# Optimization experiments

Hardware: AMD Instinct MI355X
Metric: run time of the kernel (lower is better)

## Reference

```python
import jax, jax.numpy as jnp
import numpy as np

T, B, D, H = 1024, 8, 1024, 16
NH = D // H  # 64, per-head width (nhid)
W_SCALE = 0.02


def setup_inputs() -> dict:
    key = jax.random.key(0)
    ks = jax.random.split(key, 10)
    return {
        "input_tensor": jax.random.normal(ks[0], (T, B, D), jnp.float32),
        "keys_vector": jax.random.normal(ks[1], (T, B, D), jnp.float32),
        "values_vector": jax.random.normal(ks[2], (T, B, D), jnp.float32),
        # per-head projection weights: [H, D, NH]
        "Wq": jax.random.normal(ks[3], (H, D, NH), jnp.float32) * W_SCALE,
        "bq": jnp.zeros((H, NH), jnp.float32),
        "Wk": jax.random.normal(ks[4], (H, D, NH), jnp.float32) * W_SCALE,
        "bk": jnp.zeros((H, NH), jnp.float32),
        "Wv": jax.random.normal(ks[5], (H, D, NH), jnp.float32) * W_SCALE,
        "bv": jnp.zeros((H, NH), jnp.float32),
        # output projection after concatenating heads
        "Wo": jax.random.normal(ks[6], (D, D), jnp.float32) * W_SCALE,
        "bo": jnp.zeros((D,), jnp.float32),
        "mask": 1,  # True: causal (growing key slice per timestep)
    }


def reference(input_tensor, keys_vector, values_vector, Wq, bq, Wk, bk, Wv, bv, Wo, bo, mask):
    # Vectorized equivalent of the per-timestep loop: query at step t attends
    # to keys/values[:t+1] when mask is set, else to the full sequence.
    q = jnp.einsum('tbd,hdk->tbhk', input_tensor, Wq) + bq   # [T,B,H,NH]
    k = jnp.einsum('sbd,hdk->sbhk', keys_vector, Wk) + bk    # [T,B,H,NH]
    v = jnp.einsum('sbd,hdk->sbhk', values_vector, Wv) + bv  # [T,B,H,NH]

    scale = 1.0 / jnp.sqrt(jnp.float32(NH))
    scores = jnp.einsum('tbhk,sbhk->bhts', q, k) * scale     # [B,H,T,T]
    if mask:
        causal = jnp.tril(jnp.ones((T, T), dtype=bool))      # s <= t
        scores = jnp.where(causal[None, None], scores, jnp.float32(-1e9))
    attn = jax.nn.softmax(scores, axis=-1)                   # over key dim s

    out = jnp.einsum('bhts,sbhk->tbhk', attn, v)             # [T,B,H,NH]
    out = out.reshape(T, B, D)                               # concat heads
    return out @ Wo.T + bo                                   # [T,B,D]
```

## Files before the change

### kernel.cpp

```cpp
#include <hip/hip_runtime.h>

typedef short bf16x8 __attribute__((ext_vector_type(8)));
typedef float f32x4 __attribute__((ext_vector_type(4)));
typedef float f32x16 __attribute__((ext_vector_type(16)));

typedef const __attribute__((address_space(1))) void* gptr_t;
typedef __attribute__((address_space(3))) void* sptr_t;

#define Z16 {0.f,0.f,0.f,0.f,0.f,0.f,0.f,0.f,0.f,0.f,0.f,0.f,0.f,0.f,0.f,0.f}
#define VMCNT(n) asm volatile("s_waitcnt vmcnt(" #n ")" ::: "memory")
#define LGKM0 asm volatile("s_waitcnt lgkmcnt(0)" ::: "memory")
#define SCHEDB __builtin_amdgcn_sched_barrier(0)
#define SBAR __builtin_amdgcn_s_barrier()

__device__ __forceinline__ void glds16(const void* g, void* s) {
  __builtin_amdgcn_global_load_lds((gptr_t)g, (sptr_t)s, 16, 0, 0);
}

__device__ __forceinline__ unsigned short f2bf(float x) {
  unsigned u = __float_as_uint(x);
  u = u + 0x7fffu + ((u >> 16) & 1u);
  return (unsigned short)(u >> 16);
}

__device__ __forceinline__ unsigned packbf(float lo, float hi) {
  return (unsigned)f2bf(lo) | (((unsigned)f2bf(hi)) << 16);
}

__global__ __launch_bounds__(256) void prep(const float* __restrict__ X,
                                            const float* __restrict__ KY,
                                            const float* __restrict__ VY,
                                            const float* __restrict__ Wo,
                                            const float* __restrict__ Wq,
                                            const float* __restrict__ Wk,
                                            const float* __restrict__ Wv,
                                            unsigned short* __restrict__ XB,
                                            unsigned short* __restrict__ WOB,
                                            unsigned short* __restrict__ WT) {
  __shared__ float tile[64][65];
  if (blockIdx.x < 2048) {
    int stride = 2048 * 256;
    for (int i = blockIdx.x * 256 + threadIdx.x; i < 6553600; i += stride) {
      const float* in; unsigned short* out; int k;
      if (i < 2097152)      { in = X;  out = XB;            k = i; }
      else if (i < 4194304) { in = KY; out = XB + 8388608;  k = i - 2097152; }
      else if (i < 6291456) { in = VY; out = XB + 16777216; k = i - 4194304; }
      else                  { in = Wo; out = WOB;           k = i - 6291456; }
      float4 v = ((const float4*)in)[k];
      uint2 r;
      r.x = packbf(v.x, v.y);
      r.y = packbf(v.z, v.w);
      ((uint2*)out)[k] = r;
    }
    return;
  }
  int idx = blockIdx.x - 2048;
  int bx = idx & 15, by = idx >> 4;
  int m = by >> 4, h = by & 15, d0 = bx * 64;
  const float* src = (m == 0 ? Wq : (m == 1 ? Wk : Wv)) + (size_t)h * 65536;
  int c = (threadIdx.x & 15) * 4, r0 = threadIdx.x >> 4;
#pragma unroll
  for (int rr = 0; rr < 4; ++rr) {
    int dr = rr * 16 + r0;
    float4 v = *(const float4*)(src + (size_t)(d0 + dr) * 64 + c);
    tile[dr][c + 0] = v.x; tile[dr][c + 1] = v.y;
    tile[dr][c + 2] = v.z; tile[dr][c + 3] = v.w;
  }
  __syncthreads();
#pragma unroll
  for (int rr = 0; rr < 4; ++rr) {
    int kr = rr * 16 + r0;
    uint2 pk;
    pk.x = packbf(tile[c + 0][kr], tile[c + 1][kr]);
    pk.y = packbf(tile[c + 2][kr], tile[c + 3][kr]);
    *(uint2*)(WT + ((size_t)(m * 1024 + h * 64 + kr)) * 1024 + d0 + c) = pk;
  }
}

__global__ __launch_bounds__(256) void gemm_qkv(const unsigned short* __restrict__ Ab,
                                                const unsigned short* __restrict__ Bb,
                                                const float* __restrict__ bi0,
                                                const float* __restrict__ bi1,
                                                const float* __restrict__ bi2,
                                                unsigned short* __restrict__ outp) {
  const int K = 1024;
  int z = blockIdx.z;
  const unsigned short* A = Ab + (size_t)z * 8192 * 1024;
  const unsigned short* BT = Bb + (size_t)z * 1024 * 1024;
  const float* bias = z == 0 ? bi0 : (z == 1 ? bi1 : bi2);
  int lin = blockIdx.y * 64 + blockIdx.x;
  int mt = (lin & 7) * 8 + ((lin >> 3) & 7);
  int nt = lin >> 6;
  int m0 = mt * 128, n0 = nt * 128;
  __shared__ __align__(16) char lds[65536];
  int tid = threadIdx.x, w = tid >> 6, l = tid & 63, ml = l & 15, hi = l >> 4;
  int wr = (w >> 1) * 64, wc = (w & 1) * 64;
  int srow = l >> 3;
  int kphys = (l & 7) << 4;
  f32x4 acc[4][4] = {};
#pragma unroll
  for (int i = 0; i < 4; ++i) {
    int c = w * 4 + i;
    int row = c * 8 + srow;
    int klog = kphys ^ ((row & 7) << 4);
    glds16((const char*)(A + (size_t)(m0 + row) * K) + klog, lds + c * 1024);
    glds16((const char*)(BT + (size_t)(n0 + row) * K) + klog, lds + 16384 + c * 1024);
  }
  __syncthreads();
  int cur = 0;
  for (int kt16 = 0; kt16 < 16; ++kt16) {
    if (kt16 + 1 < 16) {
      char* nb = lds + (cur ^ 1) * 32768;
      int kt = (kt16 + 1) * 64;
#pragma unroll
      for (int i = 0; i < 4; ++i) {
        int c = w * 4 + i;
        int row = c * 8 + srow;
        int klog = kphys ^ ((row & 7) << 4);
        glds16((const char*)(A + (size_t)(m0 + row) * K + kt) + klog, nb + c * 1024);
        glds16((const char*)(BT + (size_t)(n0 + row) * K + kt) + klog, nb + 16384 + c * 1024);
      }
    }
    char* As = lds + cur * 32768;
    char* Bs = As + 16384;
#pragma unroll
    for (int ks = 0; ks < 2; ++ks) {
      bf16x8 af[4], bfr[4];
#pragma unroll
      for (int mi = 0; mi < 4; ++mi) {
        int row = wr + mi * 16 + ml;
        af[mi] = *(const bf16x8*)(As + row * 128 + ((ks * 64 + (hi << 4)) ^ ((row & 7) << 4)));
      }
#pragma unroll
      for (int ni = 0; ni < 4; ++ni) {
        int row = wc + ni * 16 + ml;
        bfr[ni] = *(const bf16x8*)(Bs + row * 128 + ((ks * 64 + (hi << 4)) ^ ((row & 7) << 4)));
      }
      __builtin_amdgcn_s_setprio(1);
#pragma unroll
      for (int mi = 0; mi < 4; ++mi)
#pragma unroll
        for (int ni = 0; ni < 4; ++ni)
          acc[mi][ni] = __builtin_amdgcn_mfma_f32_16x16x32_bf16(af[mi], bfr[ni], acc[mi][ni], 0, 0, 0);
      __builtin_amdgcn_s_setprio(0);
    }
    __syncthreads();
    cur ^= 1;
  }
#pragma unroll
  for (int mi = 0; mi < 4; ++mi) {
#pragma unroll
    for (int ni = 0; ni < 4; ++ni) {
      int col = wc + ni * 16 + ml;
      float bv = bias[n0 + col];
#pragma unroll
      for (int r = 0; r < 4; ++r) {
        int row = wr + mi * 16 + (hi << 2) + r;
        float v = acc[mi][ni][r] + bv;
        float pv = __shfl_xor(v, 1);
        unsigned pk = (ml & 1) ? packbf(pv, v) : packbf(v, pv);
        *(unsigned*)(lds + row * 256 + (((col * 2) & ~3) ^ ((row & 7) << 4))) = pk;
      }
    }
  }
  __syncthreads();
  unsigned short* ob = outp + (size_t)z * 8388608;
  if (z != 2) {
    int rr = tid >> 1, hh = tid & 1;
    int t = (m0 + rr) >> 3, b = (m0 + rr) & 7;
    int hg = (n0 >> 6) + hh;
    unsigned short* dst = ob + (size_t)(b * 16 + hg) * 65536 + (size_t)t * 64;
#pragma unroll
    for (int j = 0; j < 8; ++j) {
      uint4 d = *(uint4*)(lds + rr * 256 + ((hh * 128 + j * 16) ^ ((rr & 7) << 4)));
      *(uint4*)(dst + j * 8) = d;
    }
  } else {
    int t0 = m0 >> 3;
#pragma unroll
    for (int q = 0; q < 4; ++q) {
      int run = q * 256 + tid;
      int k = run & 63;
      int bh2 = run >> 6;
      int b = bh2 >> 1, hh = bh2 & 1;
      int colb = (hh * 64 + k) * 2;
      union { unsigned short u[16]; uint4 v[2]; } tmp;
#pragma unroll
      for (int tp = 0; tp < 16; ++tp) {
        int rowt = tp * 8 + b;
        tmp.u[tp] = *(unsigned short*)(lds + rowt * 256 + (colb ^ ((b & 7) << 4)));
      }
      int hg = (n0 >> 6) + hh;
      unsigned short* dst = ob + (size_t)(b * 16 + hg) * 65536 + (size_t)k * 1024 + t0;
      *(uint4*)dst = tmp.v[0];
      *(uint4*)(dst + 8) = tmp.v[1];
    }
  }
}

__global__ __launch_bounds__(256) void gemm_out(const unsigned short* __restrict__ A,
                                                const unsigned short* __restrict__ BT,
                                                const float* __restrict__ bias,
                                                float* __restrict__ outp) {
  const int K = 1024;
  int lin = blockIdx.y * 64 + blockIdx.x;
  int mt = (lin & 7) * 8 + ((lin >> 3) & 7);
  int nt = lin >> 6;
  int m0 = mt * 128, n0 = nt * 128;
  __shared__ __align__(16) char lds[65536];
  int tid = threadIdx.x, w = tid >> 6, l = tid & 63, ml = l & 15, hi = l >> 4;
  int wr = (w >> 1) * 64, wc = (w & 1) * 64;
  int srow = l >> 3;
  int kphys = (l & 7) << 4;
  f32x4 acc[4][4] = {};
#pragma unroll
  for (int i = 0; i < 4; ++i) {
    int c = w * 4 + i;
    int row = c * 8 + srow;
    int klog = kphys ^ ((row & 7) << 4);
    glds16((const char*)(A + (size_t)(m0 + row) * K) + klog, lds + c * 1024);
    glds16((const char*)(BT + (size_t)(n0 + row) * K) + klog, lds + 16384 + c * 1024);
  }
  __syncthreads();
  int cur = 0;
  for (int kt16 = 0; kt16 < 16; ++kt16) {
    if (kt16 + 1 < 16) {
      char* nb = lds + (cur ^ 1) * 32768;
      int kt = (kt16 + 1) * 64;
#pragma unroll
      for (int i = 0; i < 4; ++i) {
        int c = w * 4 + i;
        int row = c * 8 + srow;
        int klog = kphys ^ ((row & 7) << 4);
        glds16((const char*)(A + (size_t)(m0 + row) * K + kt) + klog, nb + c * 1024);
        glds16((const char*)(BT + (size_t)(n0 + row) * K + kt) + klog, nb + 16384 + c * 1024);
      }
    }
    char* As = lds + cur * 32768;
    char* Bs = As + 16384;
#pragma unroll
    for (int ks = 0; ks < 2; ++ks) {
      bf16x8 af[4], bfr[4];
#pragma unroll
      for (int mi = 0; mi < 4; ++mi) {
        int row = wr + mi * 16 + ml;
        af[mi] = *(const bf16x8*)(As + row * 128 + ((ks * 64 + (hi << 4)) ^ ((row & 7) << 4)));
      }
#pragma unroll
      for (int ni = 0; ni < 4; ++ni) {
        int row = wc + ni * 16 + ml;
        bfr[ni] = *(const bf16x8*)(Bs + row * 128 + ((ks * 64 + (hi << 4)) ^ ((row & 7) << 4)));
      }
      __builtin_amdgcn_s_setprio(1);
#pragma unroll
      for (int mi = 0; mi < 4; ++mi)
#pragma unroll
        for (int ni = 0; ni < 4; ++ni)
          acc[mi][ni] = __builtin_amdgcn_mfma_f32_16x16x32_bf16(af[mi], bfr[ni], acc[mi][ni], 0, 0, 0);
      __builtin_amdgcn_s_setprio(0);
    }
    __syncthreads();
    cur ^= 1;
  }
#pragma unroll
  for (int mi = 0; mi < 4; ++mi) {
#pragma unroll
    for (int ni = 0; ni < 4; ++ni) {
      int col = n0 + wc + ni * 16 + ml;
      float bv = bias[col];
#pragma unroll
      for (int r = 0; r < 4; ++r) {
        int row = m0 + wr + mi * 16 + (hi << 2) + r;
        outp[(size_t)row * 1024 + col] = acc[mi][ni][r] + bv;
      }
    }
  }
}

__global__ __launch_bounds__(128, 2) void attn_k(const unsigned short* __restrict__ Qp,
                                                 const unsigned short* __restrict__ Kp,
                                                 const unsigned short* __restrict__ VTp,
                                                 unsigned short* __restrict__ Op,
                                                 const int* __restrict__ maskp) {
  int lin = blockIdx.x;
  int xcd = lin & 7, idx = lin >> 3;
  int bh = xcd + 8 * (idx & 15);
  int s = 15 - (idx >> 4);
  const size_t base = (size_t)bh * 65536;
  int tid = threadIdx.x, w = tid >> 6, l = tid & 63;
  int ml5 = l & 31, hi1 = l >> 5;
  int tw0 = s * 64 + w * 32;
  int t_glob = tw0 + ml5;
  __shared__ __align__(16) char lds[32768];
  int msk = *maskp;
  const float CE = 0.18033688011112042f;
  bf16x8 bq[4];
#pragma unroll
  for (int kd = 0; kd < 4; ++kd)
    bq[kd] = *(const bf16x8*)(Qp + base + (size_t)t_glob * 64 + kd * 16 + hi1 * 8);
  f32x16 o0 = Z16, o1 = Z16;
  float m_run = -3e38f, l_run = 0.f;
  int lim = msk ? s : 15;
  int srow = l >> 3, kphys = (l & 7) << 4;
  int klog = kphys ^ (srow << 4);
  int swz = (ml5 & 7) << 4;
  if (w == 0) {
#pragma unroll
    for (int i = 0; i < 8; ++i) {
      int row = i * 8 + srow;
      glds16((const char*)(Kp + base + (size_t)row * 64) + klog, lds + i * 1024);
    }
  } else {
#pragma unroll
    for (int i = 0; i < 8; ++i) {
      int row = i * 8 + srow;
      glds16((const char*)(VTp + base + (size_t)row * 1024) + klog, lds + 8192 + i * 1024);
    }
  }
  int cur = 0;
  for (int st = 0; st <= lim; ++st) {
    if (st < lim) {
      char* nb = lds + (cur ^ 1) * 16384;
      if (w == 0) {
#pragma unroll
        for (int i = 0; i < 8; ++i) {
          int row = i * 8 + srow;
          glds16((const char*)(Kp + base + (size_t)((st + 1) * 64 + row) * 64) + klog, nb + i * 1024);
        }
      } else {
#pragma unroll
        for (int i = 0; i < 8; ++i) {
          int row = i * 8 + srow;
          glds16((const char*)(VTp + base + (size_t)row * 1024 + (st + 1) * 64) + klog, nb + 8192 + i * 1024);
        }
      }
      VMCNT(8);
    } else {
      VMCNT(0);
    }
    SCHEDB; SBAR; SCHEDB;
    char* Ks = lds + cur * 16384;
    char* Vs = Ks + 8192;
    f32x16 s0 = Z16, s1 = Z16;
    __builtin_amdgcn_s_setprio(1);
#pragma unroll
    for (int kd = 0; kd < 4; ++kd) {
      int koff = kd * 32 + hi1 * 16;
      bf16x8 a0 = *(const bf16x8*)(Ks + ml5 * 128 + (koff ^ swz));
      bf16x8 a1 = *(const bf16x8*)(Ks + (32 + ml5) * 128 + (koff ^ swz));
      s0 = __builtin_amdgcn_mfma_f32_32x32x16_bf16(a0, bq[kd], s0, 0, 0, 0);
      s1 = __builtin_amdgcn_mfma_f32_32x32x16_bf16(a1, bq[kd], s1, 0, 0, 0);
    }
    __builtin_amdgcn_s_setprio(0);
    if (msk && st == s) {
#pragma unroll
      for (int r = 0; r < 16; ++r) {
        int sl = st * 64 + (r & 3) + 8 * (r >> 2) + 4 * hi1;
        if (sl > t_glob) s0[r] = -1e30f;
        if (sl + 32 > t_glob) s1[r] = -1e30f;
      }
    }
    float t8[8];
#pragma unroll
    for (int r = 0; r < 8; ++r)
      t8[r] = fmaxf(fmaxf(s0[r], s0[r + 8]), fmaxf(s1[r], s1[r + 8]));
    float tm = fmaxf(fmaxf(fmaxf(t8[0], t8[1]), fmaxf(t8[2], t8[3])),
                     fmaxf(fmaxf(t8[4], t8[5]), fmaxf(t8[6], t8[7])));
    tm = fmaxf(tm, __shfl_xor(tm, 32));
    if (!__all(tm <= m_run + 8.0f)) {
      float m_new = fmaxf(m_run, tm);
      float sc2 = exp2f((m_run - m_new) * CE);
      l_run *= sc2;
#pragma unroll
      for (int r = 0; r < 16; ++r) { o0[r] *= sc2; o1[r] *= sc2; }
      m_run = m_new;
    }
    float mC = m_run * CE;
#pragma unroll
    for (int r = 0; r < 16; ++r) {
      s0[r] = exp2f(fmaf(s0[r], CE, -mC));
      s1[r] = exp2f(fmaf(s1[r], CE, -mC));
    }
    float a8[8];
#pragma unroll
    for (int r = 0; r < 8; ++r)
      a8[r] = (s0[r] + s0[r + 8]) + (s1[r] + s1[r + 8]);
    float ps = ((a8[0] + a8[1]) + (a8[2] + a8[3])) + ((a8[4] + a8[5]) + (a8[6] + a8[7]));
    ps += __shfl_xor(ps, 32);
    l_run += ps;
    unsigned cc0[4][2], cc1[4][2];
#pragma unroll
    for (int q = 0; q < 4; ++q) {
      cc0[q][0] = packbf(s0[4 * q + 0], s0[4 * q + 1]);
      cc0[q][1] = packbf(s0[4 * q + 2], s0[4 * q + 3]);
      cc1[q][0] = packbf(s1[4 * q + 0], s1[4 * q + 1]);
      cc1[q][1] = packbf(s1[4 * q + 2], s1[4 * q + 3]);
    }
#define CCa(a, p) ((a) < 4 ? cc0[(a) & 3][p] : cc1[(a) & 3][p])
    union U4 { unsigned u[4]; bf16x8 v; };
    bf16x8 pb[4];
#pragma unroll
    for (int kb = 0; kb < 4; ++kb) {
      U4 t;
#pragma unroll
      for (int p = 0; p < 2; ++p) {
        unsigned x = CCa(2 * kb, p), y = CCa(2 * kb + 1, p);
        unsigned v = hi1 ? x : y;
        unsigned wv = hi1 ? y : x;
        unsigned vs = __shfl_xor(v, 32);
        t.u[p]     = hi1 ? vs : wv;
        t.u[2 + p] = hi1 ? wv : vs;
      }
      pb[kb] = t.v;
    }
#undef CCa
    __builtin_amdgcn_s_setprio(1);
#pragma unroll
    for (int kb = 0; kb < 4; ++kb) {
      int koff = kb * 32 + hi1 * 16;
      bf16x8 v0 = *(const bf16x8*)(Vs + ml5 * 128 + (koff ^ swz));
      bf16x8 v1 = *(const bf16x8*)(Vs + (32 + ml5) * 128 + (koff ^ swz));
      o0 = __builtin_amdgcn_mfma_f32_32x32x16_bf16(v0, pb[kb], o0, 0, 0, 0);
      o1 = __builtin_amdgcn_mfma_f32_32x32x16_bf16(v1, pb[kb], o1, 0, 0, 0);
    }
    __builtin_amdgcn_s_setprio(0);
    SCHEDB; LGKM0; SBAR;
    cur ^= 1;
  }
  float rl = 1.0f / l_run;
  int b = bh >> 4, h = bh & 15;
  unsigned short* orow = Op + (size_t)(t_glob * 8 + b) * 1024 + h * 64;
#pragma unroll
  for (int q2 = 0; q2 < 4; ++q2) {
    uint2 pk0, pk1;
    pk0.x = packbf(o0[4 * q2 + 0] * rl, o0[4 * q2 + 1] * rl);
    pk0.y = packbf(o0[4 * q2 + 2] * rl, o0[4 * q2 + 3] * rl);
    *(uint2*)(orow + 4 * hi1 + 8 * q2) = pk0;
    pk1.x = packbf(o1[4 * q2 + 0] * rl, o1[4 * q2 + 1] * rl);
    pk1.y = packbf(o1[4 * q2 + 2] * rl, o1[4 * q2 + 3] * rl);
    *(uint2*)(orow + 32 + 4 * hi1 + 8 * q2) = pk1;
  }
}

extern "C" void kernel_launch(void* const* d_in, const int* in_sizes, int n_in,
                              void* d_out, int out_size, void* d_ws, size_t ws_size,
                              hipStream_t stream) {
  const float* X  = (const float*)d_in[0];
  const float* KY = (const float*)d_in[1];
  const float* VY = (const float*)d_in[2];
  const float* Wq = (const float*)d_in[3];
  const float* bq = (const float*)d_in[4];
  const float* Wk = (const float*)d_in[5];
  const float* bk = (const float*)d_in[6];
  const float* Wv = (const float*)d_in[7];
  const float* bv = (const float*)d_in[8];
  const float* Wo = (const float*)d_in[9];
  const float* bo = (const float*)d_in[10];
  const int* mask = (const int*)d_in[11];
  char* ws = (char*)d_ws;
  unsigned short* XB  = (unsigned short*)(ws);
  unsigned short* WT  = (unsigned short*)(ws + 48ll * 1024 * 1024);
  unsigned short* WOB = (unsigned short*)(ws + 54ll * 1024 * 1024);
  unsigned short* QP  = (unsigned short*)(ws + 56ll * 1024 * 1024);
  unsigned short* OP  = (unsigned short*)(ws + 104ll * 1024 * 1024);

  prep<<<2816, 256, 0, stream>>>(X, KY, VY, Wo, Wq, Wk, Wv, XB, WOB, WT);
  gemm_qkv<<<dim3(64, 8, 3), 256, 0, stream>>>(XB, WT, bq, bk, bv, QP);
  attn_k<<<2048, 128, 0, stream>>>(QP, QP + 8388608, QP + 16777216, OP, mask);
  gemm_out<<<dim3(64, 8, 1), 256, 0, stream>>>(OP, WOB, bo, (float*)d_out);
}
```

Baseline: 185.5 us.

## Rewrite QKV GEMM as 256x256 tile, 8-wave, half-tile staged pipeline

Replaces the 128x128, 4-wave, double-buffered QKV projection GEMM with a 256x256 tile using 8 waves and 128 KB of dynamic LDS. Loads are split into half-tile stages that are interleaved with four MFMA quadrants, using explicit vmcnt and lgkmcnt waits and barriers so global-to-LDS prefetch overlaps compute. Larger tiles raise data reuse per LDS byte. The cost is only 384 blocks, lower occupancy and more barriers per K step. The epilogue is rescaled to the wider tile.

```diff
diff --git a/kernel.cpp b/kernel.cpp
--- a/kernel.cpp
+++ b/kernel.cpp
@@ -77,123 +77,164 @@
   }
 }
 
-__global__ __launch_bounds__(256) void gemm_qkv(const unsigned short* __restrict__ Ab,
-                                                const unsigned short* __restrict__ Bb,
-                                                const float* __restrict__ bi0,
-                                                const float* __restrict__ bi1,
-                                                const float* __restrict__ bi2,
-                                                unsigned short* __restrict__ outp) {
+__global__ __launch_bounds__(512, 2) void gemm_qkv8(const unsigned short* __restrict__ Ab,
+                                                    const unsigned short* __restrict__ Bb,
+                                                    const float* __restrict__ bi0,
+                                                    const float* __restrict__ bi1,
+                                                    const float* __restrict__ bi2,
+                                                    unsigned short* __restrict__ outp) {
+  extern __shared__ __align__(16) char lds[];
   const int K = 1024;
   int z = blockIdx.z;
   const unsigned short* A = Ab + (size_t)z * 8192 * 1024;
   const unsigned short* BT = Bb + (size_t)z * 1024 * 1024;
   const float* bias = z == 0 ? bi0 : (z == 1 ? bi1 : bi2);
-  int lin = blockIdx.y * 64 + blockIdx.x;
-  int mt = (lin & 7) * 8 + ((lin >> 3) & 7);
-  int nt = lin >> 6;
-  int m0 = mt * 128, n0 = nt * 128;
-  __shared__ __align__(16) char lds[65536];
-  int tid = threadIdx.x, w = tid >> 6, l = tid & 63, ml = l & 15, hi = l >> 4;
-  int wr = (w >> 1) * 64, wc = (w & 1) * 64;
+  int m0 = blockIdx.x * 256, n0 = blockIdx.y * 256;
+  int tid = threadIdx.x, wid = tid >> 6, l = tid & 63, ml = l & 15, hi = l >> 4;
+  int wr = (wid >> 2) * 128, wc = (wid & 3) * 64;
   int srow = l >> 3;
-  int kphys = (l & 7) << 4;
-  f32x4 acc[4][4] = {};
-#pragma unroll
-  for (int i = 0; i < 4; ++i) {
-    int c = w * 4 + i;
-    int row = c * 8 + srow;
-    int klog = kphys ^ ((row & 7) << 4);
-    glds16((const char*)(A + (size_t)(m0 + row) * K) + klog, lds + c * 1024);
-    glds16((const char*)(BT + (size_t)(n0 + row) * K) + klog, lds + 16384 + c * 1024);
+  int ksw = ((l & 7) << 4) ^ (srow << 4);
+  f32x4 acc[8][4] = {};
+  auto STG = [&](int mat, int h, int T, int d) {
+    const unsigned short* src = mat ? BT : A;
+    int rc0 = mat ? n0 : m0;
+    char* dst = lds + d * 65536 + mat * 32768 + h * 16384;
+#pragma unroll
+    for (int i = 0; i < 2; ++i) {
+      int c = wid * 2 + i;
+      int row = h * 128 + c * 8 + srow;
+      glds16((const char*)(src + (size_t)(rc0 + row) * K + T * 64) + ksw, dst + c * 1024);
+    }
+  };
+  auto RDA = [&](bf16x8 (&af)[4][2], int mg, int d) {
+    char* As = lds + d * 65536;
+#pragma unroll
+    for (int mf = 0; mf < 4; ++mf)
+#pragma unroll
+      for (int ks = 0; ks < 2; ++ks) {
+        int row = wr + mg * 64 + mf * 16 + ml;
+        af[mf][ks] = *(const bf16x8*)(As + row * 128 + ((ks * 64 + (hi << 4)) ^ ((row & 7) << 4)));
+      }
+  };
+  auto RDB = [&](bf16x8 (&bf)[2][2], int ng, int d) {
+    char* Bs = lds + d * 65536 + 32768;
+#pragma unroll
+    for (int nf = 0; nf < 2; ++nf)
+#pragma unroll
+      for (int ks = 0; ks < 2; ++ks) {
+        int row = wc + ng * 32 + nf * 16 + ml;
+        bf[nf][ks] = *(const bf16x8*)(Bs + row * 128 + ((ks * 64 + (hi << 4)) ^ ((row & 7) << 4)));
+      }
+  };
+  auto MM = [&](bf16x8 (&af)[4][2], bf16x8 (&bf)[2][2], int mg, int ng) {
+    __builtin_amdgcn_s_setprio(1);
+#pragma unroll
+    for (int ks = 0; ks < 2; ++ks)
+#pragma unroll
+      for (int mf = 0; mf < 4; ++mf)
+#pragma unroll
+        for (int nf = 0; nf < 2; ++nf)
+          acc[mg * 4 + mf][ng * 2 + nf] = __builtin_amdgcn_mfma_f32_16x16x32_bf16(
+              af[mf][ks], bf[nf][ks], acc[mg * 4 + mf][ng * 2 + nf], 0, 0, 0);
+    __builtin_amdgcn_s_setprio(0);
+  };
+  STG(0, 0, 0, 0); STG(0, 1, 0, 0); STG(1, 0, 0, 0); STG(1, 1, 0, 0);
+  STG(1, 0, 1, 1); STG(1, 1, 1, 1);
+  VMCNT(4); SCHEDB; SBAR;
+  for (int j = 0; j < 8; ++j) {
+    int b = 2 * j + 1, T2 = 2 * j + 2, T3 = 2 * j + 3;
+    bool s2 = T2 < 16, s3 = T3 < 16;
+    bf16x8 a03[4][2], a47[4][2], b01[2][2], b23[2][2];
+    RDA(a03, 0, 0); RDB(b01, 0, 0);
+    STG(0, 0, b, 1);
+    SCHEDB; SBAR; LGKM0; SCHEDB;
+    MM(a03, b01, 0, 0);
+    SCHEDB; SBAR;
+    RDB(b23, 1, 0);
+    STG(0, 1, b, 1);
+    SCHEDB; SBAR; LGKM0; SCHEDB;
+    MM(a03, b23, 0, 1);
+    SCHEDB; SBAR;
+    RDA(a47, 1, 0);
+    if (s2) STG(1, 0, T2, 0);
+    SCHEDB; SBAR; LGKM0; SCHEDB;
+    MM(a47, b23, 1, 1);
+    SCHEDB; SBAR;
+    if (s2) STG(1, 1, T2, 0);
+    SCHEDB; SBAR; LGKM0; SCHEDB;
+    MM(a47, b01, 1, 0);
+    if (j < 7) { VMCNT(4); } else { VMCNT(0); }
+    SCHEDB; SBAR;
+    RDA(a03, 0, 1); RDB(b01, 0, 1);
+    if (s2) STG(0, 0, T2, 0);
+    SCHEDB; SBAR; LGKM0; SCHEDB;
+    MM(a03, b01, 0, 0);
+    SCHEDB; SBAR;
+    RDB(b23, 1, 1);
+    if (s2) STG(0, 1, T2, 0);
+    SCHEDB; SBAR; LGKM0; SCHEDB;
+    MM(a03, b23, 0, 1);
+    SCHEDB; SBAR;
+    RDA(a47, 1, 1);
+    if (s3) STG(1, 0, T3, 1);
+    SCHEDB; SBAR; LGKM0; SCHEDB;
+    MM(a47, b23, 1, 1);
+    SCHEDB; SBAR;
+    if (s3) STG(1, 1, T3, 1);
+    SCHEDB; SBAR; LGKM0; SCHEDB;
+    MM(a47, b01, 1, 0);
+    if (j < 7) { VMCNT(4); } else { VMCNT(0); }
+    SCHEDB; SBAR;
   }
   __syncthreads();
-  int cur = 0;
-  for (int kt16 = 0; kt16 < 16; ++kt16) {
-    if (kt16 + 1 < 16) {
-      char* nb = lds + (cur ^ 1) * 32768;
-      int kt = (kt16 + 1) * 64;
-#pragma unroll
-      for (int i = 0; i < 4; ++i) {
-        int c = w * 4 + i;
-        int row = c * 8 + srow;
-        int klog = kphys ^ ((row & 7) << 4);
-        glds16((const char*)(A + (size_t)(m0 + row) * K + kt) + klog, nb + c * 1024);
-        glds16((const char*)(BT + (size_t)(n0 + row) * K + kt) + klog, nb + 16384 + c * 1024);
-      }
-    }
-    char* As = lds + cur * 32768;
-    char* Bs = As + 16384;
-#pragma unroll
-    for (int ks = 0; ks < 2; ++ks) {
-      bf16x8 af[4], bfr[4];
-#pragma unroll
-      for (int mi = 0; mi < 4; ++mi) {
-        int row = wr + mi * 16 + ml;
-        af[mi] = *(const bf16x8*)(As + row * 128 + ((ks * 64 + (hi << 4)) ^ ((row & 7) << 4)));
-      }
-#pragma unroll
-      for (int ni = 0; ni < 4; ++ni) {
-        int row = wc + ni * 16 + ml;
-        bfr[ni] = *(const bf16x8*)(Bs + row * 128 + ((ks * 64 + (hi << 4)) ^ ((row & 7) << 4)));
-      }
-      __builtin_amdgcn_s_setprio(1);
-#pragma unroll
-      for (int mi = 0; mi < 4; ++mi)
-#pragma unroll
-        for (int ni = 0; ni < 4; ++ni)
-          acc[mi][ni] = __builtin_amdgcn_mfma_f32_16x16x32_bf16(af[mi], bfr[ni], acc[mi][ni], 0, 0, 0);
-      __builtin_amdgcn_s_setprio(0);
-    }
-    __syncthreads();
-    cur ^= 1;
-  }
-#pragma unroll
-  for (int mi = 0; mi < 4; ++mi) {
-#pragma unroll
-    for (int ni = 0; ni < 4; ++ni) {
-      int col = wc + ni * 16 + ml;
-      float bv = bias[n0 + col];
+#pragma unroll
+  for (int nf = 0; nf < 4; ++nf) {
+    int col = wc + nf * 16 + ml;
+    float bv = bias[n0 + col];
+#pragma unroll
+    for (int mf = 0; mf < 8; ++mf)
 #pragma unroll
       for (int r = 0; r < 4; ++r) {
-        int row = wr + mi * 16 + (hi << 2) + r;
-        float v = acc[mi][ni][r] + bv;
+        int row = wr + mf * 16 + (hi << 2) + r;
+        float v = acc[mf][nf][r] + bv;
         float pv = __shfl_xor(v, 1);
         unsigned pk = (ml & 1) ? packbf(pv, v) : packbf(v, pv);
-        *(unsigned*)(lds + row * 256 + (((col * 2) & ~3) ^ ((row & 7) << 4))) = pk;
-      }
-    }
+        *(unsigned*)(lds + row * 512 + (((col * 2) & ~3) ^ ((row & 7) << 4))) = pk;
+      }
   }
   __syncthreads();
   unsigned short* ob = outp + (size_t)z * 8388608;
   if (z != 2) {
-    int rr = tid >> 1, hh = tid & 1;
-    int t = (m0 + rr) >> 3, b = (m0 + rr) & 7;
-    int hg = (n0 >> 6) + hh;
-    unsigned short* dst = ob + (size_t)(b * 16 + hg) * 65536 + (size_t)t * 64;
-#pragma unroll
-    for (int j = 0; j < 8; ++j) {
-      uint4 d = *(uint4*)(lds + rr * 256 + ((hh * 128 + j * 16) ^ ((rr & 7) << 4)));
-      *(uint4*)(dst + j * 8) = d;
+#pragma unroll
+    for (int q = 0; q < 2; ++q) {
+      int id = q * 512 + tid;
+      int rr = id >> 2, hh = id & 3;
+      int t = (m0 + rr) >> 3, b2 = (m0 + rr) & 7;
+      int h = (n0 >> 6) + hh;
+      unsigned short* dst = ob + (size_t)(b2 * 16 + h) * 65536 + (size_t)t * 64;
+#pragma unroll
+      for (int jj = 0; jj < 8; ++jj) {
+        uint4 d = *(uint4*)(lds + rr * 512 + ((hh * 128 + jj * 16) ^ ((rr & 7) << 4)));
+        *(uint4*)(dst + jj * 8) = d;
+      }
     }
   } else {
     int t0 = m0 >> 3;
 #pragma unroll
     for (int q = 0; q < 4; ++q) {
-      int run = q * 256 + tid;
-      int k = run & 63;
-      int bh2 = run >> 6;
-      int b = bh2 >> 1, hh = bh2 & 1;
+      int id = q * 512 + tid;
+      int k = id & 63;
+      int bh2 = id >> 6;
+      int b2 = bh2 >> 2, hh = bh2 & 3;
       int colb = (hh * 64 + k) * 2;
-      union { unsigned short u[16]; uint4 v[2]; } tmp;
-#pragma unroll
-      for (int tp = 0; tp < 16; ++tp) {
-        int rowt = tp * 8 + b;
-        tmp.u[tp] = *(unsigned short*)(lds + rowt * 256 + (colb ^ ((b & 7) << 4)));
-      }
-      int hg = (n0 >> 6) + hh;
-      unsigned short* dst = ob + (size_t)(b * 16 + hg) * 65536 + (size_t)k * 1024 + t0;
-      *(uint4*)dst = tmp.v[0];
-      *(uint4*)(dst + 8) = tmp.v[1];
+      union { unsigned short u[32]; uint4 v[4]; } tmp;
+#pragma unroll
+      for (int tp = 0; tp < 32; ++tp)
+        tmp.u[tp] = *(unsigned short*)(lds + (tp * 8 + b2) * 512 + (colb ^ (b2 << 4)));
+      int h = (n0 >> 6) + hh;
+      unsigned short* dst = ob + (size_t)(b2 * 16 + h) * 65536 + (size_t)k * 1024 + t0;
+#pragma unroll
+      for (int jj = 0; jj < 4; ++jj) *(uint4*)(dst + jj * 8) = tmp.v[jj];
     }
   }
 }
@@ -465,7 +506,7 @@
   unsigned short* OP  = (unsigned short*)(ws + 104ll * 1024 * 1024);
 
   prep<<<2816, 256, 0, stream>>>(X, KY, VY, Wo, Wq, Wk, Wv, XB, WOB, WT);
-  gemm_qkv<<<dim3(64, 8, 3), 256, 0, stream>>>(XB, WT, bq, bk, bv, QP);
+  gemm_qkv8<<<dim3(32, 4, 3), 512, 131072, stream>>>(XB, WT, bq, bk, bv, QP);
   attn_k<<<2048, 128, 0, stream>>>(QP, QP + 8388608, QP + 16777216, OP, mask);
   gemm_out<<<dim3(64, 8, 1), 256, 0, stream>>>(OP, WOB, bo, (float*)d_out);
 }
```

Result: slower. 259.3 us (+39.8%).
